# Optimization experiments

Measured on AMD Instinct MI355X. Metric: run time of the kernel, lower is better.

The kernel has to match this reference:

```python
import jax, jax.numpy as jnp
import numpy as np

C = 256   # num_channels
H = 16    # num_heads
L = 16384 # protein length
W = 15    # window (odd -> same-length conv with pad=(W-1)//2)


def setup_inputs() -> dict:
    key = jax.random.key(0)
    k = jax.random.split(key, 5)
    x = jax.random.normal(k[0], (1, C, L), dtype=jnp.float32)
    w_heads = jax.random.normal(k[1], (H, C, W), dtype=jnp.float32) * (1.0 / np.sqrt(C * W))
    b_heads = jax.random.normal(k[2], (H,), dtype=jnp.float32) * 0.01
    # grouped 1x1 conv with groups=H: per-head [C_out, C_in] matrices
    w_tr = jax.random.normal(k[3], (H, C, C), dtype=jnp.float32) * (1.0 / np.sqrt(C))
    b_tr = jax.random.normal(k[4], (H, C), dtype=jnp.float32) * 0.01
    return {"x": x, "w_heads": w_heads, "b_heads": b_heads, "w_tr": w_tr, "b_tr": b_tr}


def reference(x, w_heads, b_heads, w_tr, b_tr):
    pad = (W - 1) // 2
    # conv_heads: Conv1d(C -> H, kernel W, pad (W-1)//2)  -> scores [1, H, L]
    scores = jax.lax.conv_general_dilated(
        x, w_heads, window_strides=(1,), padding=[(pad, pad)],
        dimension_numbers=("NCH", "OIH", "NCH"),
    ) + b_heads[None, :, None]
    # batchwise softmax over sequence (single protein in batch -> softmax over L)
    focuses = jax.nn.softmax(scores, axis=-1)  # [1, H, L]
    # outer product: [1, H, 1, L] * [1, 1, C, L] -> [1, H, C, L] (the big intermediate)
    focused = focuses[:, :, None, :] * x[:, None, :, :]
    # grouped 1x1 conv (per-head CxC matmul) then sum over heads -> [1, C, L]
    out = jnp.einsum("hoc,bhcl->bol", w_tr, focused)
    out = out + jnp.sum(b_tr, axis=0)[None, :, None]  # head-summed per-group bias
    return out
```

## Files before the change

### kernel.cpp

```cpp
#include <hip/hip_runtime.h>
#include <hip/hip_bf16.h>

#define L_LEN 16384
#define C_CH  256
#define H_HEADS 16
#define W_WIN 15

typedef __attribute__((ext_vector_type(8))) short bf16x8;
typedef __attribute__((ext_vector_type(4))) float f32x4;
typedef unsigned short ushort_t;


__device__ __forceinline__ void gll16(const void* g, void* l) {
    __builtin_amdgcn_global_load_lds(
        (const __attribute__((address_space(1))) void*)g,
        (__attribute__((address_space(3))) void*)l, 16, 0, 0);
}

__device__ __forceinline__ ushort_t f2bf(float f) {
    __hip_bfloat16 b = __float2bfloat16(f);
    return *(ushort_t*)&b;
}

__global__ __launch_bounds__(256) void k_transpose(const float* __restrict__ x,
                                                   ushort_t* __restrict__ xb) {
    __shared__ float tile[64][65];
    int t = threadIdx.x;
    int l0 = blockIdx.x * 64;
    int c0 = blockIdx.y * 64;
#pragma unroll
    for (int r = 0; r < 16; ++r) {
        int c = r * 4 + (t >> 6);
        int l = t & 63;
        tile[c][l] = x[(size_t)(c0 + c) * L_LEN + l0 + l];
    }
    __syncthreads();
    int l = t >> 2;
    int cq = (t & 3) * 16;
    ushort_t tmp[16];
#pragma unroll
    for (int i = 0; i < 16; ++i) tmp[i] = f2bf(tile[cq + i][l]);
    ushort_t* dst = xb + (size_t)(l0 + l) * C_CH + c0 + cq;
    *(uint4*)dst = *(uint4*)&tmp[0];
    *(uint4*)(dst + 8) = *(uint4*)&tmp[8];
}

__global__ __launch_bounds__(256) void k_aconv(const float* __restrict__ wtr,
                                               ushort_t* __restrict__ Ag) {
    int tid = blockIdx.x * 256 + threadIdx.x;
    int base = tid * 8;
    int m = base >> 12;
    int k = base & 4095;
    int h = k >> 8, c = k & 255;
    const float* src = wtr + ((size_t)h * C_CH + m) * C_CH + c;
    ushort_t tmp[8];
#pragma unroll
    for (int i = 0; i < 8; ++i) tmp[i] = f2bf(src[i]);
    *(uint4*)(Ag + base) = *(uint4*)tmp;
}

__global__ void k_bias(const float* __restrict__ btr, float* __restrict__ bias) {
    int o = threadIdx.x;
    float s = 0.f;
#pragma unroll
    for (int h = 0; h < H_HEADS; ++h) s += btr[h * C_CH + o];
    bias[o] = s;
}

__global__ __launch_bounds__(256) void k_wprep(const float* __restrict__ wh,
                                               ushort_t* __restrict__ awf) {
    int tid = blockIdx.x * 256 + threadIdx.x;
    int e = tid & 7;
    int lane = (tid >> 3) & 63;
    int ktw = tid >> 9;
    int w = ktw >> 3, kt = ktw & 7;
    int h = lane & 15;
    int c = kt * 32 + (lane >> 4) * 8 + e;
    awf[tid] = f2bf(wh[((size_t)h * C_CH + c) * W_WIN + w]);
}

__global__ __launch_bounds__(128) void k_convm(const ushort_t* __restrict__ xb,
                                               const ushort_t* __restrict__ awf,
                                               float* __restrict__ scores) {
    __shared__ char xs[48 * 512];
    int t = threadIdx.x;
    int n0 = blockIdx.x * 32;
#pragma unroll
    for (int i = 0; i < 12; ++i) {
        int chunk = t + i * 128;
        int rr = chunk >> 5;
        int cb = (chunk & 31) * 16;
        int l = n0 - 8 + rr;
        uint4 v = {0u, 0u, 0u, 0u};
        if (l >= 0 && l < L_LEN) v = *(const uint4*)(xb + (size_t)l * C_CH + (cb >> 1));
        *(uint4*)(&xs[rr * 512 + (cb ^ ((rr & 7) << 4))]) = v;
    }
    __syncthreads();
    int wv = t >> 6, lane = t & 63;
    int r = lane & 15, q = lane >> 4;
    const f32x4 vzero = {0.f, 0.f, 0.f, 0.f};
    f32x4 acc[4] = {vzero, vzero, vzero, vzero};
    for (int w = 0; w < 15; ++w) {
        int rr = wv * 16 + r + w + 1;
        const char* rowp = &xs[rr * 512];
        int sw = (rr & 7) << 4;
#pragma unroll
        for (int kt = 0; kt < 8; ++kt) {
            bf16x8 a = *(const bf16x8*)(awf + (size_t)(((w * 8 + kt) * 64 + lane) * 8));
            bf16x8 b = *(const bf16x8*)(rowp + ((kt * 64 + q * 16) ^ sw));
            acc[kt & 3] = __builtin_amdgcn_mfma_f32_16x16x32_bf16(a, b, acc[kt & 3], 0, 0, 0);
        }
    }
    f32x4 s = acc[0] + acc[1] + acc[2] + acc[3];
    int nb = n0 + wv * 16;
#pragma unroll
    for (int e = 0; e < 4; ++e)
        scores[(size_t)(q * 4 + e) * L_LEN + nb + r] = s[e];
}

__global__ __launch_bounds__(1024) void k_softmax(float* __restrict__ scfoc,
                                                  const float* __restrict__ bh) {
    __shared__ float red[17];
    int h = blockIdx.x, t = threadIdx.x;
    int wid = t >> 6, ln = t & 63;
    float b = bh[h];
    float s[16];
#pragma unroll
    for (int r = 0; r < 16; ++r)
        s[r] = b + scfoc[(size_t)h * L_LEN + r * 1024 + t];
    float mx = s[0];
#pragma unroll
    for (int r = 1; r < 16; ++r) mx = fmaxf(mx, s[r]);
    for (int o = 32; o > 0; o >>= 1) mx = fmaxf(mx, __shfl_xor(mx, o));
    if (ln == 0) red[wid] = mx;
    __syncthreads();
    if (t == 0) {
        float m2 = red[0];
        for (int i = 1; i < 16; ++i) m2 = fmaxf(m2, red[i]);
        red[16] = m2;
    }
    __syncthreads();
    float M = red[16];
    float sum = 0.f;
#pragma unroll
    for (int r = 0; r < 16; ++r) {
        float e = __expf(s[r] - M);
        s[r] = e;
        sum += e;
    }
    for (int o = 32; o > 0; o >>= 1) sum += __shfl_xor(sum, o);
    __syncthreads();
    if (ln == 0) red[wid] = sum;
    __syncthreads();
    if (t == 0) {
        float s2 = 0.f;
        for (int i = 0; i < 16; ++i) s2 += red[i];
        red[16] = s2;
    }
    __syncthreads();
    float inv = 1.0f / red[16];
#pragma unroll
    for (int r = 0; r < 16; ++r)
        scfoc[(size_t)h * L_LEN + r * 1024 + t] = s[r] * inv;
}

#define GLDSA 16384
#define GBUF  32768

__global__ __launch_bounds__(256, 2) void k_gemm(const ushort_t* __restrict__ Ag,
                                                 const ushort_t* __restrict__ xb,
                                                 const float* __restrict__ foc,
                                                 const float* __restrict__ bias,
                                                 float* __restrict__ out) {
    __shared__ char lds[2 * GBUF];
    int t = threadIdx.x;
    int w = t >> 6, lane = t & 63;
    int m0 = blockIdx.y * 128, n0 = blockIdx.x * 128;
    int wr = w >> 1, wc = w & 1;
    int r = lane & 15, q = lane >> 4;

    const f32x4 vzero = {0.f, 0.f, 0.f, 0.f};
    f32x4 oacc[4][4], hacc[4][4];
#pragma unroll
    for (int i = 0; i < 4; ++i)
#pragma unroll
        for (int j = 0; j < 4; ++j) { oacc[i][j] = vzero; hacc[i][j] = vzero; }

    auto stageA = [&](int buf, int kt) {
        const ushort_t* s = Ag + (size_t)(m0 + (t >> 3)) * 4096 + kt * 64 + (t & 7) * 8;
        char* base = lds + buf * GBUF + (w << 10);
#pragma unroll
        for (int j = 0; j < 4; ++j)
            gll16(s + (size_t)j * 32 * 4096, base + j * 4096);
    };
    auto stageB = [&](int buf, int kt) {
        int kc = (kt & 3) * 64;
        const ushort_t* s = xb + (size_t)(n0 + (t >> 3)) * 256 + kc + (t & 7) * 8;
        char* base = lds + buf * GBUF + GLDSA + (w << 10);
#pragma unroll
        for (int j = 0; j < 4; ++j)
            gll16(s + (size_t)j * 32 * 256, base + j * 4096);
    };
    auto compute = [&](int buf) {
        char* Ab = lds + buf * GBUF;
        char* Bb = Ab + GLDSA;
#pragma unroll
        for (int kk = 0; kk < 2; ++kk) {
            bf16x8 a[4], bfr[4];
#pragma unroll
            for (int i = 0; i < 4; ++i)
                a[i] = *(const bf16x8*)(Ab + (wr * 64 + i * 16 + r) * 128 + kk * 64 + q * 16);
#pragma unroll
            for (int j = 0; j < 4; ++j)
                bfr[j] = *(const bf16x8*)(Bb + (wc * 64 + j * 16 + r) * 128 + kk * 64 + q * 16);
#pragma unroll
            for (int i = 0; i < 4; ++i)
#pragma unroll
                for (int j = 0; j < 4; ++j)
                    hacc[i][j] = __builtin_amdgcn_mfma_f32_16x16x32_bf16(a[i], bfr[j], hacc[i][j], 0, 0, 0);
        }
    };

    stageA(0, 0);
    stageB(0, 0);
    __syncthreads();

    for (int h = 0; h < H_HEADS; ++h) {
        float f[4];
#pragma unroll
        for (int j = 0; j < 4; ++j)
            f[j] = foc[(size_t)h * L_LEN + n0 + wc * 64 + j * 16 + r];
#pragma unroll
        for (int qq = 0; qq < 4; ++qq) {
            int kt = h * 4 + qq;
            int buf = qq & 1;
            if (kt < 63) { stageA(buf ^ 1, kt + 1); stageB(buf ^ 1, kt + 1); }
            compute(buf);
            __syncthreads();
        }
#pragma unroll
        for (int i = 0; i < 4; ++i)
#pragma unroll
            for (int j = 0; j < 4; ++j) {
                oacc[i][j] += hacc[i][j] * f[j];
                hacc[i][j] = vzero;
            }
    }

#pragma unroll
    for (int i = 0; i < 4; ++i) {
        int mrow = m0 + wr * 64 + i * 16 + q * 4;
        float4 bv = *(const float4*)&bias[mrow];
        float bvr[4] = {bv.x, bv.y, bv.z, bv.w};
#pragma unroll
        for (int j = 0; j < 4; ++j) {
            int n = n0 + wc * 64 + j * 16 + r;
#pragma unroll
            for (int rr = 0; rr < 4; ++rr)
                out[(size_t)(mrow + rr) * L_LEN + n] = oacc[i][j][rr] + bvr[rr];
        }
    }
}

extern "C" void kernel_launch(void* const* d_in, const int* in_sizes, int n_in,
                              void* d_out, int out_size, void* d_ws, size_t ws_size,
                              hipStream_t stream) {
    const float* x   = (const float*)d_in[0];
    const float* wh  = (const float*)d_in[1];
    const float* bh  = (const float*)d_in[2];
    const float* wtr = (const float*)d_in[3];
    const float* btr = (const float*)d_in[4];
    float* out = (float*)d_out;
    char* ws = (char*)d_ws;

    ushort_t* Ag    = (ushort_t*)(ws);
    ushort_t* xb    = (ushort_t*)(ws + ((size_t)2 << 20));
    float*    scfoc = (float*)(ws + ((size_t)10 << 20));
    float*    bias  = (float*)(ws + ((size_t)11 << 20));
    ushort_t* awf   = (ushort_t*)(ws + ((size_t)11 << 20) + 4096);

    k_transpose<<<dim3(256, 4), 256, 0, stream>>>(x, xb);
    k_aconv<<<dim3(512), 256, 0, stream>>>(wtr, Ag);
    k_bias<<<1, 256, 0, stream>>>(btr, bias);
    k_wprep<<<dim3(240), 256, 0, stream>>>(wh, awf);
    k_convm<<<dim3(512), 128, 0, stream>>>(xb, awf, scfoc);
    k_softmax<<<16, 1024, 0, stream>>>(scfoc, bh);
    k_gemm<<<dim3(128, 2), 256, 0, stream>>>(Ag, xb, scfoc, bias, out);
}
```

Baseline: 149.1 us.

## Split softmax into partial reductions, fuse normalization into GEMM, keep B resident

The single-pass softmax (16 blocks) becomes a 128-block partial max/sum reduction plus a tiny combine kernel, which also absorbs the bias sum. The exp and normalize step moves into the GEMM's focus-weight load. The GEMM now loads its whole 128x256 bf16 x tile into LDS once and streams only the weight tiles. xb and Ag are written to global memory in an XOR-swizzled layout so the LDS reads stay conflict-free. The conv kernel uses direct global-to-LDS loads with clamped rows that are then zeroed at the edges. In exchange, the GEMM's larger LDS footprint limits it to one block per CU, and the per-head score bias is dropped, which is valid because softmax is shift-invariant.

```diff
diff --git a/kernel.cpp b/kernel.cpp
--- a/kernel.cpp
+++ b/kernel.cpp
@@ -40,31 +40,28 @@
     ushort_t tmp[16];
 #pragma unroll
     for (int i = 0; i < 16; ++i) tmp[i] = f2bf(tile[cq + i][l]);
-    ushort_t* dst = xb + (size_t)(l0 + l) * C_CH + c0 + cq;
-    *(uint4*)dst = *(uint4*)&tmp[0];
-    *(uint4*)(dst + 8) = *(uint4*)&tmp[8];
+    char* rowp = (char*)(xb + (size_t)(l0 + l) * C_CH);
+    int swz = (l & 7) << 4;
+    int b0 = (c0 + cq) * 2;
+    *(uint4*)(rowp + (b0 ^ swz)) = *(uint4*)&tmp[0];
+    *(uint4*)(rowp + ((b0 + 16) ^ swz)) = *(uint4*)&tmp[8];
 }
 
 __global__ __launch_bounds__(256) void k_aconv(const float* __restrict__ wtr,
                                                ushort_t* __restrict__ Ag) {
     int tid = blockIdx.x * 256 + threadIdx.x;
-    int base = tid * 8;
-    int m = base >> 12;
-    int k = base & 4095;
-    int h = k >> 8, c = k & 255;
+    size_t D = (size_t)tid * 16;
+    int m = (int)(D >> 13);
+    int inner = (int)(D & 8191);
+    int kt = inner >> 7, wb = inner & 127;
+    int ob = kt * 128 + (wb ^ ((m & 7) << 4));
+    int k0 = ob >> 1;
+    int h = k0 >> 8, c = k0 & 255;
     const float* src = wtr + ((size_t)h * C_CH + m) * C_CH + c;
     ushort_t tmp[8];
 #pragma unroll
     for (int i = 0; i < 8; ++i) tmp[i] = f2bf(src[i]);
-    *(uint4*)(Ag + base) = *(uint4*)tmp;
-}
-
-__global__ void k_bias(const float* __restrict__ btr, float* __restrict__ bias) {
-    int o = threadIdx.x;
-    float s = 0.f;
-#pragma unroll
-    for (int h = 0; h < H_HEADS; ++h) s += btr[h * C_CH + o];
-    bias[o] = s;
+    *(uint4*)((char*)Ag + D) = *(uint4*)tmp;
 }
 
 __global__ __launch_bounds__(256) void k_wprep(const float* __restrict__ wh,
@@ -91,11 +88,20 @@
         int rr = chunk >> 5;
         int cb = (chunk & 31) * 16;
         int l = n0 - 8 + rr;
-        uint4 v = {0u, 0u, 0u, 0u};
-        if (l >= 0 && l < L_LEN) v = *(const uint4*)(xb + (size_t)l * C_CH + (cb >> 1));
-        *(uint4*)(&xs[rr * 512 + (cb ^ ((rr & 7) << 4))]) = v;
-    }
-    __syncthreads();
+        int lc = l < 0 ? 0 : (l >= L_LEN ? L_LEN - 1 : l);
+        gll16((const char*)xb + (size_t)lc * 512 + cb, xs + chunk * 16);
+    }
+    __syncthreads();
+    if (n0 == 0 || n0 == L_LEN - 32) {
+        int rbase = (n0 == 0) ? 0 : 40;
+        uint4 z = {0u, 0u, 0u, 0u};
+#pragma unroll
+        for (int i = 0; i < 2; ++i) {
+            int ch = t + i * 128;
+            *(uint4*)(xs + rbase * 512 + ch * 16) = z;
+        }
+        __syncthreads();
+    }
     int wv = t >> 6, lane = t & 63;
     int r = lane & 15, q = lane >> 4;
     const f32x4 vzero = {0.f, 0.f, 0.f, 0.f};
@@ -118,67 +124,95 @@
         scores[(size_t)(q * 4 + e) * L_LEN + nb + r] = s[e];
 }
 
-__global__ __launch_bounds__(1024) void k_softmax(float* __restrict__ scfoc,
-                                                  const float* __restrict__ bh) {
-    __shared__ float red[17];
-    int h = blockIdx.x, t = threadIdx.x;
-    int wid = t >> 6, ln = t & 63;
-    float b = bh[h];
-    float s[16];
-#pragma unroll
-    for (int r = 0; r < 16; ++r)
-        s[r] = b + scfoc[(size_t)h * L_LEN + r * 1024 + t];
-    float mx = s[0];
-#pragma unroll
-    for (int r = 1; r < 16; ++r) mx = fmaxf(mx, s[r]);
+__global__ __launch_bounds__(256) void k_smred(const float* __restrict__ scores,
+                                               float* __restrict__ mpart,
+                                               float* __restrict__ zpart) {
+    __shared__ float red[8];
+    int b = blockIdx.x;
+    int h = b >> 3, seg = b & 7;
+    int t = threadIdx.x, wid = t >> 6, ln = t & 63;
+    const float* sp = scores + (size_t)h * L_LEN + seg * 2048;
+    float v[8];
+    float mx = -1e30f;
+#pragma unroll
+    for (int i = 0; i < 8; ++i) {
+        v[i] = sp[i * 256 + t];
+        mx = fmaxf(mx, v[i]);
+    }
     for (int o = 32; o > 0; o >>= 1) mx = fmaxf(mx, __shfl_xor(mx, o));
     if (ln == 0) red[wid] = mx;
     __syncthreads();
     if (t == 0) {
-        float m2 = red[0];
-        for (int i = 1; i < 16; ++i) m2 = fmaxf(m2, red[i]);
-        red[16] = m2;
-    }
-    __syncthreads();
-    float M = red[16];
-    float sum = 0.f;
-#pragma unroll
-    for (int r = 0; r < 16; ++r) {
-        float e = __expf(s[r] - M);
-        s[r] = e;
-        sum += e;
-    }
-    for (int o = 32; o > 0; o >>= 1) sum += __shfl_xor(sum, o);
-    __syncthreads();
-    if (ln == 0) red[wid] = sum;
+        float m2 = fmaxf(fmaxf(red[0], red[1]), fmaxf(red[2], red[3]));
+        red[4] = m2;
+    }
+    __syncthreads();
+    float M = red[4];
+    float s = 0.f;
+#pragma unroll
+    for (int i = 0; i < 8; ++i) s += __expf(v[i] - M);
+    for (int o = 32; o > 0; o >>= 1) s += __shfl_xor(s, o);
+    if (ln == 0) red[wid] = s;
     __syncthreads();
     if (t == 0) {
-        float s2 = 0.f;
-        for (int i = 0; i < 16; ++i) s2 += red[i];
-        red[16] = s2;
-    }
-    __syncthreads();
-    float inv = 1.0f / red[16];
-#pragma unroll
-    for (int r = 0; r < 16; ++r)
-        scfoc[(size_t)h * L_LEN + r * 1024 + t] = s[r] * inv;
-}
-
-#define GLDSA 16384
-#define GBUF  32768
-
-__global__ __launch_bounds__(256, 2) void k_gemm(const ushort_t* __restrict__ Ag,
+        mpart[b] = M;
+        zpart[b] = red[0] + red[1] + red[2] + red[3];
+    }
+}
+
+__global__ void k_scalars(const float* __restrict__ btr,
+                          const float* __restrict__ mpart,
+                          const float* __restrict__ zpart,
+                          float* __restrict__ bias,
+                          float2* __restrict__ MZ) {
+    int t = threadIdx.x;
+    float s = 0.f;
+#pragma unroll
+    for (int h = 0; h < H_HEADS; ++h) s += btr[h * C_CH + t];
+    bias[t] = s;
+    if (t < H_HEADS) {
+        float M = -1e30f;
+#pragma unroll
+        for (int g = 0; g < 8; ++g) M = fmaxf(M, mpart[t * 8 + g]);
+        float Z = 0.f;
+#pragma unroll
+        for (int g = 0; g < 8; ++g) Z += zpart[t * 8 + g] * __expf(mpart[t * 8 + g] - M);
+        float2 r; r.x = M; r.y = 1.0f / Z;
+        MZ[t] = r;
+    }
+}
+
+#define BRES 65536
+#define ATS  16384
+
+__global__ __launch_bounds__(256, 1) void k_gemm(const ushort_t* __restrict__ Ag,
                                                  const ushort_t* __restrict__ xb,
-                                                 const float* __restrict__ foc,
+                                                 const float* __restrict__ scores,
+                                                 const float2* __restrict__ MZ,
                                                  const float* __restrict__ bias,
                                                  float* __restrict__ out) {
-    __shared__ char lds[2 * GBUF];
+    __shared__ char lds[BRES + 2 * ATS];
     int t = threadIdx.x;
     int w = t >> 6, lane = t & 63;
     int m0 = blockIdx.y * 128, n0 = blockIdx.x * 128;
     int wr = w >> 1, wc = w & 1;
     int r = lane & 15, q = lane >> 4;
 
+#pragma unroll
+    for (int i = 0; i < 16; ++i) {
+        int chunk = t + i * 256;
+        int row = chunk >> 5, cb = (chunk & 31) * 16;
+        gll16((const char*)xb + (size_t)(n0 + row) * 512 + cb, lds + chunk * 16);
+    }
+    auto stageA = [&](int buf, int kt) {
+        const char* src = (const char*)Ag + (size_t)(m0 + (t >> 3)) * 8192 + kt * 128 + (t & 7) * 16;
+        char* dst = lds + BRES + buf * ATS + t * 16;
+#pragma unroll
+        for (int j = 0; j < 4; ++j)
+            gll16(src + (size_t)j * 32 * 8192, dst + j * 4096);
+    };
+    stageA(0, 0);
+
     const f32x4 vzero = {0.f, 0.f, 0.f, 0.f};
     f32x4 oacc[4][4], hacc[4][4];
 #pragma unroll
@@ -186,56 +220,42 @@
 #pragma unroll
         for (int j = 0; j < 4; ++j) { oacc[i][j] = vzero; hacc[i][j] = vzero; }
 
-    auto stageA = [&](int buf, int kt) {
-        const ushort_t* s = Ag + (size_t)(m0 + (t >> 3)) * 4096 + kt * 64 + (t & 7) * 8;
-        char* base = lds + buf * GBUF + (w << 10);
-#pragma unroll
-        for (int j = 0; j < 4; ++j)
-            gll16(s + (size_t)j * 32 * 4096, base + j * 4096);
-    };
-    auto stageB = [&](int buf, int kt) {
-        int kc = (kt & 3) * 64;
-        const ushort_t* s = xb + (size_t)(n0 + (t >> 3)) * 256 + kc + (t & 7) * 8;
-        char* base = lds + buf * GBUF + GLDSA + (w << 10);
-#pragma unroll
-        for (int j = 0; j < 4; ++j)
-            gll16(s + (size_t)j * 32 * 256, base + j * 4096);
-    };
-    auto compute = [&](int buf) {
-        char* Ab = lds + buf * GBUF;
-        char* Bb = Ab + GLDSA;
-#pragma unroll
-        for (int kk = 0; kk < 2; ++kk) {
-            bf16x8 a[4], bfr[4];
-#pragma unroll
-            for (int i = 0; i < 4; ++i)
-                a[i] = *(const bf16x8*)(Ab + (wr * 64 + i * 16 + r) * 128 + kk * 64 + q * 16);
-#pragma unroll
-            for (int j = 0; j < 4; ++j)
-                bfr[j] = *(const bf16x8*)(Bb + (wc * 64 + j * 16 + r) * 128 + kk * 64 + q * 16);
-#pragma unroll
-            for (int i = 0; i < 4; ++i)
-#pragma unroll
-                for (int j = 0; j < 4; ++j)
-                    hacc[i][j] = __builtin_amdgcn_mfma_f32_16x16x32_bf16(a[i], bfr[j], hacc[i][j], 0, 0, 0);
-        }
-    };
-
-    stageA(0, 0);
-    stageB(0, 0);
     __syncthreads();
 
     for (int h = 0; h < H_HEADS; ++h) {
+        float2 mz = MZ[h];
         float f[4];
 #pragma unroll
-        for (int j = 0; j < 4; ++j)
-            f[j] = foc[(size_t)h * L_LEN + n0 + wc * 64 + j * 16 + r];
+        for (int j = 0; j < 4; ++j) {
+            float s = scores[(size_t)h * L_LEN + n0 + wc * 64 + j * 16 + r];
+            f[j] = __expf(s - mz.x) * mz.y;
+        }
 #pragma unroll
         for (int qq = 0; qq < 4; ++qq) {
             int kt = h * 4 + qq;
-            int buf = qq & 1;
-            if (kt < 63) { stageA(buf ^ 1, kt + 1); stageB(buf ^ 1, kt + 1); }
-            compute(buf);
+            int buf = kt & 1;
+            if (kt < 63) stageA(buf ^ 1, kt + 1);
+            char* Ab = lds + BRES + buf * ATS;
+#pragma unroll
+            for (int kk = 0; kk < 2; ++kk) {
+                bf16x8 a[4], bb[4];
+#pragma unroll
+                for (int i = 0; i < 4; ++i) {
+                    int ar = wr * 64 + i * 16 + r;
+                    a[i] = *(const bf16x8*)(Ab + ar * 128 + ((kk * 64 + q * 16) ^ ((ar & 7) << 4)));
+                }
+#pragma unroll
+                for (int j = 0; j < 4; ++j) {
+                    int br = wc * 64 + j * 16 + r;
+                    bb[j] = *(const bf16x8*)(lds + br * 512 +
+                              ((qq * 128 + kk * 64 + q * 16) ^ ((br & 7) << 4)));
+                }
+#pragma unroll
+                for (int i = 0; i < 4; ++i)
+#pragma unroll
+                    for (int j = 0; j < 4; ++j)
+                        hacc[i][j] = __builtin_amdgcn_mfma_f32_16x16x32_bf16(a[i], bb[j], hacc[i][j], 0, 0, 0);
+            }
             __syncthreads();
         }
 #pragma unroll
@@ -267,23 +287,26 @@
                               hipStream_t stream) {
     const float* x   = (const float*)d_in[0];
     const float* wh  = (const float*)d_in[1];
-    const float* bh  = (const float*)d_in[2];
+    const float* btr = (const float*)d_in[4];
     const float* wtr = (const float*)d_in[3];
-    const float* btr = (const float*)d_in[4];
     float* out = (float*)d_out;
     char* ws = (char*)d_ws;
 
-    ushort_t* Ag    = (ushort_t*)(ws);
-    ushort_t* xb    = (ushort_t*)(ws + ((size_t)2 << 20));
-    float*    scfoc = (float*)(ws + ((size_t)10 << 20));
-    float*    bias  = (float*)(ws + ((size_t)11 << 20));
-    ushort_t* awf   = (ushort_t*)(ws + ((size_t)11 << 20) + 4096);
+    ushort_t* Ag     = (ushort_t*)(ws);
+    ushort_t* xb     = (ushort_t*)(ws + ((size_t)2 << 20));
+    float*    scores = (float*)(ws + ((size_t)10 << 20));
+    ushort_t* awf    = (ushort_t*)(ws + ((size_t)11 << 20));
+    char*     sc     = ws + ((size_t)11 << 20) + (128 << 10);
+    float*    mpart  = (float*)(sc);
+    float*    zpart  = (float*)(sc + 512);
+    float2*   MZ     = (float2*)(sc + 1024);
+    float*    bias   = (float*)(sc + 2048);
 
     k_transpose<<<dim3(256, 4), 256, 0, stream>>>(x, xb);
     k_aconv<<<dim3(512), 256, 0, stream>>>(wtr, Ag);
-    k_bias<<<1, 256, 0, stream>>>(btr, bias);
     k_wprep<<<dim3(240), 256, 0, stream>>>(wh, awf);
-    k_convm<<<dim3(512), 128, 0, stream>>>(xb, awf, scfoc);
-    k_softmax<<<16, 1024, 0, stream>>>(scfoc, bh);
-    k_gemm<<<dim3(128, 2), 256, 0, stream>>>(Ag, xb, scfoc, bias, out);
-}
+    k_convm<<<dim3(512), 128, 0, stream>>>(xb, awf, scores);
+    k_smred<<<dim3(128), 256, 0, stream>>>(scores, mpart, zpart);
+    k_scalars<<<1, 256, 0, stream>>>(btr, mpart, zpart, bias, MZ);
+    k_gemm<<<dim3(128, 2), 256, 0, stream>>>(Ag, xb, scores, MZ, bias, out);
+}
```

New measurement: 138.6 us. 1.08x faster.
